# Kernel optimization log

Hardware: AMD Instinct MI355X
Metric: run time of the kernel (lower is better)

Reference implementation:

```python
import jax, jax.numpy as jnp
import numpy as np

T, B, S, A, D = 512, 256, 256, 8, 64
EPS = 1e-6
LOG2PI = float(np.log(2.0 * np.pi))


def setup_inputs() -> dict:
    key = jax.random.key(0)
    ks = jax.random.split(key, 6)
    return {
        "x": jax.random.normal(ks[0], (T, B, D), dtype=jnp.float32),
        "a": jax.random.uniform(ks[1], (T, B, A), dtype=jnp.float32),
        "mask": jnp.ones((T, B), dtype=jnp.float32),
        "mu": jax.random.normal(ks[2], (S, D), dtype=jnp.float32),
        "lv": jax.random.normal(ks[3], (S, D), dtype=jnp.float32) * 0.1,
        "w_logits": jax.random.normal(ks[4], (A, S, S), dtype=jnp.float32),
        "s0_logits": jax.random.normal(ks[5], (S,), dtype=jnp.float32),
    }


def _gauss_log_prob(x, mu, lv):
    # x: [T,B,D], mu/lv: [S,D] -> [T,B,S]; diagonal Gaussian via matmul expansion
    inv_var = jnp.exp(-lv)                                  # [S,D]
    quad = (jnp.einsum('tbd,sd->tbs', x * x, inv_var)
            - 2.0 * jnp.einsum('tbd,sd->tbs', x, mu * inv_var)
            + jnp.sum(mu * mu * inv_var, axis=-1))          # [T,B,S]
    return -0.5 * (quad + jnp.sum(lv, axis=-1) + D * LOG2PI)


def reference(x, a, mask, mu, lv, w_logits, s0_logits):
    trans_all = jax.nn.softmax(w_logits, axis=-1)           # [A,S,S] row-stochastic
    log_pi0 = jax.nn.log_softmax(s0_logits)                 # [S]
    logp_x = _gauss_log_prob(x, mu, lv)                     # [T,B,S]

    # ---- forward (alpha) ----
    b1 = jax.nn.softmax(logp_x[0] + log_pi0[None, :], axis=-1)  # [B,S]

    def fstep(b, inp):
        lx, a_prev = inp
        trans = jnp.einsum('ba,aij->bij', a_prev, trans_all)      # [B,S,S]
        logp_z = jnp.log(jnp.sum(trans * b[:, :, None] + EPS, axis=1))
        b_t = jax.nn.softmax(lx + logp_z, axis=-1)
        return b_t, b_t

    _, alpha_rest = jax.lax.scan(fstep, b1, (logp_x[1:], a[:-1]))
    alpha = jnp.concatenate([b1[None], alpha_rest], axis=0)       # [T,B,S]

    # ---- backward (log beta) ----
    logb_T = jnp.zeros((B, S), dtype=x.dtype)

    def bstep(logb, inp):
        lx, a_prev, m_t = inp
        trans = jnp.einsum('ba,aij->bij', a_prev, trans_all)      # [B,S,S]
        logb_prev = jax.nn.logsumexp(lx[:, None, :] + jnp.log(trans + EPS)
                                     + logb[:, None, :], axis=-1)
        logb_prev = logb_prev * (m_t[:, None] == 1.0)
        return logb_prev, logb_prev

    _, beta_rest = jax.lax.scan(bstep, logb_T, (logp_x[1:], a[:-1], mask[1:]),
                                reverse=True)
    log_beta = jnp.concatenate([beta_rest, logb_T[None]], axis=0)  # [T,B,S]

    # ---- posterior state marginals ----
    q_z = jax.nn.softmax(jnp.log(alpha + EPS) + log_beta, axis=-1)
    return q_z
```

## Files before the change

### kernel.cpp

```cpp
#include <hip/hip_runtime.h>
#include <hip/hip_bf16.h>

#define TT 512
#define BB 256
#define SS 256
#define AA 8
#define DD 64

typedef unsigned short ushort_t;
typedef unsigned long long u64_t;
typedef __bf16 bf16x8 __attribute__((ext_vector_type(8)));
typedef float  f32x4  __attribute__((ext_vector_type(4)));
typedef unsigned int u32x4v __attribute__((ext_vector_type(4)));
typedef unsigned int u32x2v __attribute__((ext_vector_type(2)));

__device__ __forceinline__ ushort_t f2bf(float x) {
  union { float f; unsigned u; } v; v.f = x;
  unsigned r = (v.u + 0x7FFFu + ((v.u >> 16) & 1u)) >> 16;
  return (ushort_t)r;
}
__device__ __forceinline__ float bf2f(unsigned h) {
  return __uint_as_float((h & 0xFFFFu) << 16);
}
__device__ __forceinline__ void st_u32(unsigned* p, unsigned v) {
  __hip_atomic_store(p, v, __ATOMIC_RELAXED, __HIP_MEMORY_SCOPE_AGENT);
}

__device__ __forceinline__ void poll_once(const u64_t* p0, const u64_t* p1,
                                          const u64_t* pcf,
                                          u64_t d[8], unsigned& clo, unsigned& chi) {
  u32x4v a0, a1, a2, a3; u32x2v cf;
  asm volatile(
      "global_load_dwordx4 %0, %5, off sc0 sc1\n\t"
      "global_load_dwordx4 %1, %6, off sc0 sc1\n\t"
      "global_load_dwordx4 %2, %7, off sc0 sc1\n\t"
      "global_load_dwordx4 %3, %8, off sc0 sc1\n\t"
      "global_load_dwordx2 %4, %9, off sc0 sc1\n\t"
      "s_waitcnt vmcnt(0)"
      : "=&v"(a0), "=&v"(a1), "=&v"(a2), "=&v"(a3), "=&v"(cf)
      : "v"(p0), "v"(p0 + 2), "v"(p1), "v"(p1 + 2), "v"(pcf)
      : "memory");
  d[0] = (u64_t)a0[0] | ((u64_t)a0[1] << 32);
  d[1] = (u64_t)a0[2] | ((u64_t)a0[3] << 32);
  d[2] = (u64_t)a1[0] | ((u64_t)a1[1] << 32);
  d[3] = (u64_t)a1[2] | ((u64_t)a1[3] << 32);
  d[4] = (u64_t)a2[0] | ((u64_t)a2[1] << 32);
  d[5] = (u64_t)a2[2] | ((u64_t)a2[3] << 32);
  d[6] = (u64_t)a3[0] | ((u64_t)a3[1] << 32);
  d[7] = (u64_t)a3[2] | ((u64_t)a3[3] << 32);
  clo = cf[0]; chi = cf[1];
}

__global__ __launch_bounds__(64) void k_params(const float* __restrict__ mu,
                                               const float* __restrict__ lv,
                                               float* __restrict__ A1, float* __restrict__ A2,
                                               float* __restrict__ Cs) {
  const float LOG2PI = 1.8378770664093453f;
  int s = blockIdx.x, d = threadIdx.x;
  float l = lv[s * DD + d], m_ = mu[s * DD + d];
  float inv = __expf(-l);
  A1[s * DD + d] = inv;
  A2[s * DD + d] = m_ * inv;
  float part = m_ * m_ * inv + l;
  #pragma unroll
  for (int o = 32; o >= 1; o >>= 1) part += __shfl_down(part, o);
  if (d == 0) Cs[s] = part + (float)DD * LOG2PI;
}

__global__ __launch_bounds__(256) void k_pi0(const float* __restrict__ s0, float* __restrict__ lp0) {
  __shared__ float red[4];
  int tid = threadIdx.x, ln = tid & 63, wv = tid >> 6;
  float v = s0[tid];
  float m = v;
  #pragma unroll
  for (int o = 32; o >= 1; o >>= 1) m = fmaxf(m, __shfl_xor(m, o));
  if (ln == 0) red[wv] = m;
  __syncthreads();
  m = fmaxf(fmaxf(red[0], red[1]), fmaxf(red[2], red[3]));
  __syncthreads();
  float e = __expf(v - m);
  float s = e;
  #pragma unroll
  for (int o = 32; o >= 1; o >>= 1) s += __shfl_xor(s, o);
  if (ln == 0) red[wv] = s;
  __syncthreads();
  s = red[0] + red[1] + red[2] + red[3];
  lp0[tid] = v - m - __logf(s);
}

__global__ __launch_bounds__(256) void k_trans(const float* __restrict__ wl,
                                               ushort_t* __restrict__ Wf, ushort_t* __restrict__ Wb) {
  int tid = threadIdx.x;
  int rl = tid >> 5, l = tid & 31;
  int row = blockIdx.x * 8 + rl;
  int a = row >> 8, i = row & 255;
  const float* src = wl + (size_t)row * 256 + l * 8;
  float v[8];
  *reinterpret_cast<float4*>(&v[0]) = *reinterpret_cast<const float4*>(src);
  *reinterpret_cast<float4*>(&v[4]) = *reinterpret_cast<const float4*>(src + 4);
  float m = v[0];
  #pragma unroll
  for (int k = 1; k < 8; ++k) m = fmaxf(m, v[k]);
  #pragma unroll
  for (int o = 16; o >= 1; o >>= 1) m = fmaxf(m, __shfl_xor(m, o, 32));
  float s = 0.f;
  #pragma unroll
  for (int k = 0; k < 8; ++k) { v[k] = __expf(v[k] - m); s += v[k]; }
  #pragma unroll
  for (int o = 16; o >= 1; o >>= 1) s += __shfl_xor(s, o, 32);
  float inv = 1.0f / s;
  #pragma unroll
  for (int k = 0; k < 8; ++k) {
    int j = l * 8 + k;
    ushort_t h = f2bf(v[k] * inv);
    size_t fi = (size_t)((a * 8 + (i >> 5)) * 16 + (j >> 4));
    Wf[fi * 512 + (((i >> 3) & 3) * 16 + (j & 15)) * 8 + (i & 7)] = h;
    size_t bi = (size_t)((a * 8 + (j >> 5)) * 16 + (i >> 4));
    Wb[bi * 512 + (((j >> 3) & 3) * 16 + (i & 15)) * 8 + (j & 7)] = h;
  }
}

__global__ __launch_bounds__(256) void k_logp(const float* __restrict__ x,
    const float* __restrict__ A1, const float* __restrict__ A2,
    const float* __restrict__ Cs, float* __restrict__ logp, float* __restrict__ Mmax) {
  __shared__ float sA1[64][64];
  __shared__ float sA2[64][64];
  int tid = threadIdx.x;
  int row = tid >> 3, dg = tid & 7;
  size_t row0 = (size_t)blockIdx.x * 32;
  const float* xp = x + (row0 + row) * DD + dg * 8;
  float xv[8];
  *reinterpret_cast<float4*>(&xv[0]) = *reinterpret_cast<const float4*>(xp);
  *reinterpret_cast<float4*>(&xv[4]) = *reinterpret_cast<const float4*>(xp + 4);
  float m = -3.0e38f;
  float* orow = logp + (row0 + row) * SS;
  for (int st = 0; st < 4; ++st) {
    __syncthreads();
    #pragma unroll
    for (int k = 0; k < 4; ++k) {
      int flat = k * 1024 + tid * 4;
      int sr = flat >> 6, sc = flat & 63;
      *reinterpret_cast<float4*>(&sA1[sr][sc]) = *reinterpret_cast<const float4*>(&A1[(size_t)(st * 64 + sr) * 64 + sc]);
      *reinterpret_cast<float4*>(&sA2[sr][sc]) = *reinterpret_cast<const float4*>(&A2[(size_t)(st * 64 + sr) * 64 + sc]);
    }
    __syncthreads();
    for (int s = 0; s < 64; ++s) {
      float acc = 0.f;
      #pragma unroll
      for (int j = 0; j < 8; ++j) {
        float t1 = __builtin_fmaf(sA1[s][dg * 8 + j], xv[j], -2.0f * sA2[s][dg * 8 + j]);
        acc = __builtin_fmaf(t1, xv[j], acc);
      }
      acc += __shfl_xor(acc, 1, 8);
      acc += __shfl_xor(acc, 2, 8);
      acc += __shfl_xor(acc, 4, 8);
      float lp = -0.5f * (acc + Cs[st * 64 + s]);
      m = fmaxf(m, lp);
      if (((s ^ dg) & 7) == 0) orow[st * 64 + s] = lp;
    }
  }
  if (dg == 0) Mmax[row0 + row] = m;
}

__global__ __launch_bounds__(256, 1) void k_recur(
    const float* __restrict__ a_in, const float* __restrict__ mask,
    float* __restrict__ out, float* __restrict__ beta,
    const float* __restrict__ logp, const float* __restrict__ Mmax,
    float* __restrict__ cpart,
    const ushort_t* __restrict__ Wf, const ushort_t* __restrict__ Wb,
    const float* __restrict__ lp0,
    unsigned* __restrict__ amb, unsigned* __restrict__ bmb,
    unsigned* __restrict__ cmb, unsigned* __restrict__ rmb) {
  const float EPSF  = 1e-6f;
  const float EPS_S = 256.0f * 1e-6f;
  const int tid  = threadIdx.x;
  const int lane = tid & 63;
  const int wave = tid >> 6;
  const int xcd  = blockIdx.x & 7;
  const int slot = blockIdx.x >> 3;
  const int wg   = slot & 7;
  const int grpg = (slot >> 3) * 8 + xcd;
  const bool isF = (grpg < 16);
  const int grp  = grpg & 15;
  const int b0   = grp * 16;
  const int jc0  = wg * 32;

  __shared__ float yred[2][4][2][64][4];
  __shared__ float rowUp[2][4][16];

  bf16x8 bfrag[8][2][2];
  {
    const ushort_t* Ws = isF ? Wf : Wb;
    #pragma unroll
    for (int a = 0; a < 8; ++a)
      #pragma unroll
      for (int kk = 0; kk < 2; ++kk)
        #pragma unroll
        for (int nt = 0; nt < 2; ++nt) {
          const int kc = wave * 2 + kk;
          const int fragid = (a * 8 + kc) * 16 + wg * 2 + nt;
          bfrag[a][kk][nt] = *reinterpret_cast<const bf16x8*>(Ws + (size_t)fragid * 512 + lane * 8);
        }
  }

  const int m_ = lane & 15;
  const int q_ = lane >> 4;
  const int frow = tid >> 4;
  const int fcol = tid & 15;
  const int lsrc = (frow >> 2) * 16 + fcol;
  const int rg_  = frow & 3;
  const u64_t TAGMASK = 0xFFFF0000FFFF0000ULL;
  const size_t fpub = (size_t)(frow & 7) * 16 + wg * 2 + (frow >> 3);

  if (isF) {
    {
      float mm = Mmax[b0 + frow];
      float csum = 0.f;
      #pragma unroll
      for (int nt = 0; nt < 2; ++nt) {
        int j = jc0 + nt * 16 + fcol;
        float lx = logp[(size_t)(b0 + frow) * SS + j];
        float v = __expf(lx - mm + lp0[j]);
        st_u32(&amb[((size_t)(0 * 16 + grp) * 16 + frow) * 256 + j], (unsigned)f2bf(v));
        out[(size_t)(b0 + frow) * SS + j] = v;
        csum += v;
      }
      #pragma unroll
      for (int o = 8; o >= 1; o >>= 1) csum += __shfl_down(csum, o, 16);
      if (fcol == 0) {
        st_u32(&cmb[((size_t)(0 * 16 + grp)) * 128 + fpub], (unsigned)f2bf(csum));
        cpart[((size_t)grp * 16 + frow) * 8 + wg] = csum;
      }
    }

    for (int t = 1; t < TT; ++t) {
      const int par_r = (t - 1) & 1, par_w = t & 1;
      float wcur[4][8];
      {
        const float* ab = a_in + ((size_t)(t - 1) * BB + b0 + q_ * 4) * AA;
        #pragma unroll
        for (int r = 0; r < 4; ++r) {
          *reinterpret_cast<float4*>(&wcur[r][0]) = *reinterpret_cast<const float4*>(ab + r * AA);
          *reinterpret_cast<float4*>(&wcur[r][4]) = *reinterpret_cast<const float4*>(ab + r * AA + 4);
        }
      }
      float mmn = Mmax[(size_t)t * BB + b0 + frow];
      const float* lsp = logp + ((size_t)t * BB + b0 + frow) * SS + jc0;
      float ex0 = __expf(lsp[fcol] - mmn);
      float ex1 = __expf(lsp[16 + fcol] - mmn);

      const u64_t* pr = (const u64_t*)(amb + (((size_t)par_r * 16 + grp) * 16 + m_) * 256);
      const u64_t* p0 = pr + wave * 32 + q_ * 4;
      const u64_t* p1 = p0 + 16;
      const u64_t* pcf = (const u64_t*)cmb + ((size_t)par_r * 16 + grp) * 64 + (lane >> 3) * 8 + (lane & 7);
      const unsigned tg = (unsigned)(t - 1);
      const u64_t pat = ((u64_t)tg << 48) | ((u64_t)tg << 16);
      u64_t d[8]; unsigned clo, chi;
      while (true) {
        poll_once(p0, p1, pcf, d, clo, chi);
        bool ok = ((clo >> 16) == tg) & ((chi >> 16) == tg);
        #pragma unroll
        for (int k = 0; k < 8; ++k) ok &= ((d[k] & TAGMASK) == pat);
        if (__all(ok)) break;
      }
      float slo = bf2f(clo), shi = bf2f(chi);
      slo += __shfl_xor(slo, 4, 8); slo += __shfl_xor(slo, 2, 8); slo += __shfl_xor(slo, 1, 8);
      shi += __shfl_xor(shi, 4, 8); shi += __shfl_xor(shi, 2, 8); shi += __shfl_xor(shi, 1, 8);
      float vlo = __shfl(slo, (m_ & 7) * 8);
      float vhi = __shfl(shi, (m_ & 7) * 8);
      float ra = 1.0f / ((m_ < 8) ? vlo : vhi);

      float ys[2][4] = {{0.f,0.f,0.f,0.f},{0.f,0.f,0.f,0.f}};
      {
        bf16x8 af0, af1;
        #pragma unroll
        for (int e = 0; e < 8; ++e) {
          unsigned h0 = (e & 1) ? (unsigned)(d[e >> 1] >> 32) : (unsigned)d[e >> 1];
          unsigned h1 = (e & 1) ? (unsigned)(d[4 + (e >> 1)] >> 32) : (unsigned)d[4 + (e >> 1)];
          af0[e] = (__bf16)(bf2f(h0) * ra);
          af1[e] = (__bf16)(bf2f(h1) * ra);
        }
        #pragma unroll
        for (int a = 0; a < 8; ++a) {
          #pragma unroll
          for (int nt = 0; nt < 2; ++nt) {
            f32x4 c = {0.f, 0.f, 0.f, 0.f};
            c = __builtin_amdgcn_mfma_f32_16x16x32_bf16(af0, bfrag[a][0][nt], c, 0, 0, 0);
            c = __builtin_amdgcn_mfma_f32_16x16x32_bf16(af1, bfrag[a][1][nt], c, 0, 0, 0);
            #pragma unroll
            for (int r = 0; r < 4; ++r) ys[nt][r] += wcur[r][a] * c[r];
          }
        }
      }
      #pragma unroll
      for (int nt = 0; nt < 2; ++nt)
        *reinterpret_cast<float4*>(&yred[par_w][wave][nt][lane][0]) =
            make_float4(ys[nt][0], ys[nt][1], ys[nt][2], ys[nt][3]);
      __syncthreads();
      {
        float* orow = out + ((size_t)t * BB + b0 + frow) * SS + jc0;
        unsigned* mrow = amb + (((size_t)par_w * 16 + grp) * 16 + frow) * 256 + jc0;
        float y0 = yred[par_w][0][0][lsrc][rg_] + yred[par_w][1][0][lsrc][rg_] +
                   yred[par_w][2][0][lsrc][rg_] + yred[par_w][3][0][lsrc][rg_];
        float y1 = yred[par_w][0][1][lsrc][rg_] + yred[par_w][1][1][lsrc][rg_] +
                   yred[par_w][2][1][lsrc][rg_] + yred[par_w][3][1][lsrc][rg_];
        float bh0 = ex0 * (y0 + EPS_S);
        float bh1 = ex1 * (y1 + EPS_S);
        st_u32(mrow + fcol, ((unsigned)t << 16) | f2bf(bh0));
        st_u32(mrow + 16 + fcol, ((unsigned)t << 16) | f2bf(bh1));
        float csum = bh0 + bh1;
        #pragma unroll
        for (int o = 8; o >= 1; o >>= 1) csum += __shfl_down(csum, o, 16);
        if (fcol == 0)
          st_u32(&cmb[((size_t)par_w * 16 + grp) * 128 + fpub],
                 ((unsigned)t << 16) | f2bf(csum));
        orow[fcol] = bh0;
        orow[16 + fcol] = bh1;
        if (fcol == 0) {
          float cs = __shfl(csum, (tid >> 4) * 16, 64);
          cpart[(((size_t)t * 16 + grp) * 16 + frow) * 8 + wg] = cs;
        }
      }
    }
  } else {
    {
      const unsigned tg0 = (unsigned)(TT - 1);
      float* brow = beta + ((size_t)(TT - 1) * BB + b0 + frow) * SS + jc0;
      unsigned* mrow = bmb + (((size_t)((TT - 1) & 1) * 16 + grp) * 16 + frow) * 256 + jc0;
      st_u32(mrow + fcol, (tg0 << 16) | 0x3F80u);
      st_u32(mrow + 16 + fcol, (tg0 << 16) | 0x3F80u);
      brow[fcol] = 1.0f; brow[16 + fcol] = 1.0f;
      if (fcol == 0)
        st_u32(&rmb[((size_t)((TT - 1) & 1) * 16 + grp) * 128 + fpub],
               (tg0 << 16) | f2bf(32.0f));
    }

    for (int t = TT - 2; t >= 0; --t) {
      const int tr = t + 1;
      const int par_r = tr & 1, par_w = t & 1;
      float wcur[4][8];
      {
        const float* ab = a_in + ((size_t)t * BB + b0 + q_ * 4) * AA;
        #pragma unroll
        for (int r = 0; r < 4; ++r) {
          *reinterpret_cast<float4*>(&wcur[r][0]) = *reinterpret_cast<const float4*>(ab + r * AA);
          *reinterpret_cast<float4*>(&wcur[r][4]) = *reinterpret_cast<const float4*>(ab + r * AA + 4);
        }
      }
      float lp0v[8], lp1v[8];
      {
        const float* lrow = logp + ((size_t)tr * BB + b0 + m_) * SS + wave * 64 + q_ * 8;
        *reinterpret_cast<float4*>(&lp0v[0]) = *reinterpret_cast<const float4*>(lrow);
        *reinterpret_cast<float4*>(&lp0v[4]) = *reinterpret_cast<const float4*>(lrow + 4);
        *reinterpret_cast<float4*>(&lp1v[0]) = *reinterpret_cast<const float4*>(lrow + 32);
        *reinterpret_cast<float4*>(&lp1v[4]) = *reinterpret_cast<const float4*>(lrow + 36);
      }
      float mm_ = Mmax[(size_t)tr * BB + b0 + m_];
      float mk  = mask[(size_t)tr * BB + b0 + frow];

      const u64_t* pr = (const u64_t*)(bmb + (((size_t)par_r * 16 + grp) * 16 + m_) * 256);
      const u64_t* p0 = pr + wave * 32 + q_ * 4;
      const u64_t* p1 = p0 + 16;
      const u64_t* pcf = (const u64_t*)rmb + ((size_t)par_r * 16 + grp) * 64 + (lane >> 3) * 8 + (lane & 7);
      const unsigned tg = (unsigned)tr;
      const u64_t pat = ((u64_t)tg << 48) | ((u64_t)tg << 16);
      u64_t d[8]; unsigned clo, chi;
      while (true) {
        poll_once(p0, p1, pcf, d, clo, chi);
        bool ok = ((clo >> 16) == tg) & ((chi >> 16) == tg);
        #pragma unroll
        for (int k = 0; k < 8; ++k) ok &= ((d[k] & TAGMASK) == pat);
        if (__all(ok)) break;
      }
      float slo = bf2f(clo), shi = bf2f(chi);
      slo += __shfl_xor(slo, 4, 8); slo += __shfl_xor(slo, 2, 8); slo += __shfl_xor(slo, 1, 8);
      shi += __shfl_xor(shi, 4, 8); shi += __shfl_xor(shi, 2, 8); shi += __shfl_xor(shi, 1, 8);
      float vlo = __shfl(slo, (m_ & 7) * 8);
      float vhi = __shfl(shi, (m_ & 7) * 8);
      float ri = 1.0f / ((m_ < 8) ? vlo : vhi);
      float vloF = __shfl(slo, (frow & 7) * 8);
      float vhiF = __shfl(shi, (frow & 7) * 8);
      float riF = 1.0f / ((frow < 8) ? vloF : vhiF);

      float partial = 0.f;
      float ys[2][4] = {{0.f,0.f,0.f,0.f},{0.f,0.f,0.f,0.f}};
      {
        bf16x8 af0, af1;
        #pragma unroll
        for (int e = 0; e < 8; ++e) {
          unsigned h0 = (e & 1) ? (unsigned)(d[e >> 1] >> 32) : (unsigned)d[e >> 1];
          unsigned h1 = (e & 1) ? (unsigned)(d[4 + (e >> 1)] >> 32) : (unsigned)d[4 + (e >> 1)];
          float g0 = __expf(lp0v[e] - mm_) * bf2f(h0);
          float g1 = __expf(lp1v[e] - mm_) * bf2f(h1);
          partial += g0 + g1;
          af0[e] = (__bf16)(g0 * ri);
          af1[e] = (__bf16)(g1 * ri);
        }
        #pragma unroll
        for (int a = 0; a < 8; ++a) {
          #pragma unroll
          for (int nt = 0; nt < 2; ++nt) {
            f32x4 c = {0.f, 0.f, 0.f, 0.f};
            c = __builtin_amdgcn_mfma_f32_16x16x32_bf16(af0, bfrag[a][0][nt], c, 0, 0, 0);
            c = __builtin_amdgcn_mfma_f32_16x16x32_bf16(af1, bfrag[a][1][nt], c, 0, 0, 0);
            #pragma unroll
            for (int r = 0; r < 4; ++r) ys[nt][r] += wcur[r][a] * c[r];
          }
        }
      }
      partial += __shfl_xor(partial, 16);
      partial += __shfl_xor(partial, 32);
      if (q_ == 0) rowUp[par_w][wave][m_] = partial;
      #pragma unroll
      for (int nt = 0; nt < 2; ++nt)
        *reinterpret_cast<float4*>(&yred[par_w][wave][nt][lane][0]) =
            make_float4(ys[nt][0], ys[nt][1], ys[nt][2], ys[nt][3]);
      __syncthreads();
      {
        float rowU = rowUp[par_w][0][frow] + rowUp[par_w][1][frow] +
                     rowUp[par_w][2][frow] + rowUp[par_w][3][frow];
        float eg = EPSF * riF * rowU;
        bool mk1 = (mk == 1.0f);
        float* brow = beta + ((size_t)t * BB + b0 + frow) * SS + jc0;
        unsigned* mrow = bmb + (((size_t)par_w * 16 + grp) * 16 + frow) * 256 + jc0;
        float y0 = yred[par_w][0][0][lsrc][rg_] + yred[par_w][1][0][lsrc][rg_] +
                   yred[par_w][2][0][lsrc][rg_] + yred[par_w][3][0][lsrc][rg_];
        float y1 = yred[par_w][0][1][lsrc][rg_] + yred[par_w][1][1][lsrc][rg_] +
                   yred[par_w][2][1][lsrc][rg_] + yred[par_w][3][1][lsrc][rg_];
        float v0 = mk1 ? (y0 + eg) : 1.0f;
        float v1 = mk1 ? (y1 + eg) : 1.0f;
        st_u32(mrow + fcol, ((unsigned)t << 16) | f2bf(v0));
        st_u32(mrow + 16 + fcol, ((unsigned)t << 16) | f2bf(v1));
        float rsum = v0 + v1;
        #pragma unroll
        for (int o = 8; o >= 1; o >>= 1) rsum += __shfl_down(rsum, o, 16);
        if (fcol == 0)
          st_u32(&rmb[((size_t)par_w * 16 + grp) * 128 + fpub],
                 ((unsigned)t << 16) | f2bf(rsum));
        brow[fcol] = v0;
        brow[16 + fcol] = v1;
      }
    }
  }
}

__global__ __launch_bounds__(256) void k_qz(float* __restrict__ out,
    const float* __restrict__ beta, const float* __restrict__ cpart) {
  const float EPSF = 1e-6f;
  int tid = threadIdx.x;
  size_t row = (size_t)blockIdx.x * 8 + (tid >> 5);
  int l = tid & 31;
  int tt = (int)(row >> 8);
  int b  = (int)(row & 255);
  int grp = b >> 4, r = b & 15;
  float pv = 0.f;
  if (l < 8) pv = cpart[(((size_t)tt * 16 + grp) * 16 + r) * 8 + l];
  pv += __shfl_down(pv, 4, 8); pv += __shfl_down(pv, 2, 8); pv += __shfl_down(pv, 1, 8);
  float ce = __shfl(pv, 0, 32) * EPSF;
  float* po = out + row * SS + l * 8;
  const float* pb = beta + row * SS + l * 8;
  float4 v0 = *reinterpret_cast<const float4*>(po);
  float4 v1 = *reinterpret_cast<const float4*>(po + 4);
  float4 b0 = *reinterpret_cast<const float4*>(pb);
  float4 b1 = *reinterpret_cast<const float4*>(pb + 4);
  float z[8];
  z[0] = __logf(v0.x + ce) + __logf(b0.x);
  z[1] = __logf(v0.y + ce) + __logf(b0.y);
  z[2] = __logf(v0.z + ce) + __logf(b0.z);
  z[3] = __logf(v0.w + ce) + __logf(b0.w);
  z[4] = __logf(v1.x + ce) + __logf(b1.x);
  z[5] = __logf(v1.y + ce) + __logf(b1.y);
  z[6] = __logf(v1.z + ce) + __logf(b1.z);
  z[7] = __logf(v1.w + ce) + __logf(b1.w);
  float m = z[0];
  #pragma unroll
  for (int k = 1; k < 8; ++k) m = fmaxf(m, z[k]);
  #pragma unroll
  for (int o = 16; o >= 1; o >>= 1) m = fmaxf(m, __shfl_xor(m, o, 32));
  float e[8]; float s = 0.f;
  #pragma unroll
  for (int k = 0; k < 8; ++k) { e[k] = __expf(z[k] - m); s += e[k]; }
  #pragma unroll
  for (int o = 16; o >= 1; o >>= 1) s += __shfl_xor(s, o, 32);
  float inv = 1.0f / s;
  *reinterpret_cast<float4*>(po)     = make_float4(e[0]*inv, e[1]*inv, e[2]*inv, e[3]*inv);
  *reinterpret_cast<float4*>(po + 4) = make_float4(e[4]*inv, e[5]*inv, e[6]*inv, e[7]*inv);
}

extern "C" void kernel_launch(void* const* d_in, const int* in_sizes, int n_in,
                              void* d_out, int out_size, void* d_ws, size_t ws_size,
                              hipStream_t stream) {
  (void)in_sizes; (void)n_in; (void)out_size;
  const float* x   = (const float*)d_in[0];
  const float* a   = (const float*)d_in[1];
  const float* msk = (const float*)d_in[2];
  const float* mu  = (const float*)d_in[3];
  const float* lv  = (const float*)d_in[4];
  const float* wl  = (const float*)d_in[5];
  const float* s0  = (const float*)d_in[6];
  float* out = (float*)d_out;

  char* ws = (char*)d_ws;
  float* logp  = (float*)ws;  ws += (size_t)TT * BB * SS * 4;
  float* beta  = (float*)ws;  ws += (size_t)TT * BB * SS * 4;
  float* Mmax  = (float*)ws;  ws += (size_t)TT * BB * 4;
  float* cpart = (float*)ws;  ws += (size_t)TT * BB * 8 * 4;
  ushort_t* Wf = (ushort_t*)ws; ws += (size_t)AA * SS * SS * 2;
  ushort_t* Wb = (ushort_t*)ws; ws += (size_t)AA * SS * SS * 2;
  float* A1 = (float*)ws;    ws += (size_t)SS * DD * 4;
  float* A2 = (float*)ws;    ws += (size_t)SS * DD * 4;
  float* Cs = (float*)ws;    ws += 1024;
  float* lp0 = (float*)ws;   ws += 1024;
  unsigned* amb = (unsigned*)ws; ws += (size_t)2 * 16 * 16 * 256 * 4;
  unsigned* bmb = (unsigned*)ws; ws += (size_t)2 * 16 * 16 * 256 * 4;
  unsigned* cmb = (unsigned*)ws; ws += (size_t)2 * 16 * 16 * 8 * 4;
  unsigned* rmb = (unsigned*)ws; ws += (size_t)2 * 16 * 16 * 8 * 4;
  if (ws_size < (size_t)(ws - (char*)d_ws)) return;

  hipMemsetAsync(amb, 0xFF, (size_t)(2 * 16 * 16 * 256 * 4) * 2 + (size_t)(2 * 16 * 16 * 8 * 4) * 2, stream);

  k_params<<<SS, DD, 0, stream>>>(mu, lv, A1, A2, Cs);
  k_pi0<<<1, SS, 0, stream>>>(s0, lp0);
  k_trans<<<256, 256, 0, stream>>>(wl, Wf, Wb);
  k_logp<<<TT * BB / 32, 256, 0, stream>>>(x, A1, A2, Cs, logp, Mmax);
  k_recur<<<256, 256, 0, stream>>>(a, msk, out, beta, logp, Mmax, cpart, Wf, Wb, lp0,
                                   amb, bmb, cmb, rmb);
  k_qz<<<TT * BB / 8, 256, 0, stream>>>(out, beta, cpart);
}
```

Baseline: 2.076 ms.

## Defer row-sum normalization past the MFMA to take flag polling off the critical path

The recurrence loop used to poll the message data and the per-row normalization sums together, then scale the A operand before running the MFMAs. Now it polls only the data, runs the MFMAs on unscaled values, and polls the row-sum flags after the block barrier. The reciprocal is applied to the reduced output instead, in both the forward and backward chains. This aims to overlap the wait for the sums with the matrix work and to drop per-element scaling before the MFMA, at the cost of a second polling loop and a change in bf16 rounding order. The backward exp terms are also hoisted ahead of the poll, and the cmb/rmb workspace sizes were corrected (the new sizes are the same).

```diff
diff --git a/kernel.cpp b/kernel.cpp
--- a/kernel.cpp
+++ b/kernel.cpp
@@ -13,6 +13,7 @@
 typedef float  f32x4  __attribute__((ext_vector_type(4)));
 typedef unsigned int u32x4v __attribute__((ext_vector_type(4)));
 typedef unsigned int u32x2v __attribute__((ext_vector_type(2)));
+typedef short short8v __attribute__((ext_vector_type(8)));
 
 __device__ __forceinline__ ushort_t f2bf(float x) {
   union { float f; unsigned u; } v; v.f = x;
@@ -26,19 +27,16 @@
   __hip_atomic_store(p, v, __ATOMIC_RELAXED, __HIP_MEMORY_SCOPE_AGENT);
 }
 
-__device__ __forceinline__ void poll_once(const u64_t* p0, const u64_t* p1,
-                                          const u64_t* pcf,
-                                          u64_t d[8], unsigned& clo, unsigned& chi) {
-  u32x4v a0, a1, a2, a3; u32x2v cf;
+__device__ __forceinline__ void poll_data(const u64_t* p0, const u64_t* p1, u64_t d[8]) {
+  u32x4v a0, a1, a2, a3;
   asm volatile(
-      "global_load_dwordx4 %0, %5, off sc0 sc1\n\t"
-      "global_load_dwordx4 %1, %6, off sc0 sc1\n\t"
-      "global_load_dwordx4 %2, %7, off sc0 sc1\n\t"
-      "global_load_dwordx4 %3, %8, off sc0 sc1\n\t"
-      "global_load_dwordx2 %4, %9, off sc0 sc1\n\t"
+      "global_load_dwordx4 %0, %4, off sc0 sc1\n\t"
+      "global_load_dwordx4 %1, %5, off sc0 sc1\n\t"
+      "global_load_dwordx4 %2, %6, off sc0 sc1\n\t"
+      "global_load_dwordx4 %3, %7, off sc0 sc1\n\t"
       "s_waitcnt vmcnt(0)"
-      : "=&v"(a0), "=&v"(a1), "=&v"(a2), "=&v"(a3), "=&v"(cf)
-      : "v"(p0), "v"(p0 + 2), "v"(p1), "v"(p1 + 2), "v"(pcf)
+      : "=&v"(a0), "=&v"(a1), "=&v"(a2), "=&v"(a3)
+      : "v"(p0), "v"(p0 + 2), "v"(p1), "v"(p1 + 2)
       : "memory");
   d[0] = (u64_t)a0[0] | ((u64_t)a0[1] << 32);
   d[1] = (u64_t)a0[2] | ((u64_t)a0[3] << 32);
@@ -48,6 +46,13 @@
   d[5] = (u64_t)a2[2] | ((u64_t)a2[3] << 32);
   d[6] = (u64_t)a3[0] | ((u64_t)a3[1] << 32);
   d[7] = (u64_t)a3[2] | ((u64_t)a3[3] << 32);
+}
+__device__ __forceinline__ void poll_flags(const u64_t* pcf, unsigned& clo, unsigned& chi) {
+  u32x2v cf;
+  asm volatile(
+      "global_load_dwordx2 %0, %1, off sc0 sc1\n\t"
+      "s_waitcnt vmcnt(0)"
+      : "=&v"(cf) : "v"(pcf) : "memory");
   clo = cf[0]; chi = cf[1];
 }
 
@@ -255,41 +260,38 @@
       const u64_t* pcf = (const u64_t*)cmb + ((size_t)par_r * 16 + grp) * 64 + (lane >> 3) * 8 + (lane & 7);
       const unsigned tg = (unsigned)(t - 1);
       const u64_t pat = ((u64_t)tg << 48) | ((u64_t)tg << 16);
-      u64_t d[8]; unsigned clo, chi;
+      u64_t d[8];
       while (true) {
-        poll_once(p0, p1, pcf, d, clo, chi);
-        bool ok = ((clo >> 16) == tg) & ((chi >> 16) == tg);
+        poll_data(p0, p1, d);
+        bool ok = true;
         #pragma unroll
         for (int k = 0; k < 8; ++k) ok &= ((d[k] & TAGMASK) == pat);
         if (__all(ok)) break;
       }
-      float slo = bf2f(clo), shi = bf2f(chi);
-      slo += __shfl_xor(slo, 4, 8); slo += __shfl_xor(slo, 2, 8); slo += __shfl_xor(slo, 1, 8);
-      shi += __shfl_xor(shi, 4, 8); shi += __shfl_xor(shi, 2, 8); shi += __shfl_xor(shi, 1, 8);
-      float vlo = __shfl(slo, (m_ & 7) * 8);
-      float vhi = __shfl(shi, (m_ & 7) * 8);
-      float ra = 1.0f / ((m_ < 8) ? vlo : vhi);
-
-      float ys[2][4] = {{0.f,0.f,0.f,0.f},{0.f,0.f,0.f,0.f}};
+      bf16x8 af0, af1;
       {
-        bf16x8 af0, af1;
+        short8v s0v, s1v;
         #pragma unroll
         for (int e = 0; e < 8; ++e) {
           unsigned h0 = (e & 1) ? (unsigned)(d[e >> 1] >> 32) : (unsigned)d[e >> 1];
           unsigned h1 = (e & 1) ? (unsigned)(d[4 + (e >> 1)] >> 32) : (unsigned)d[4 + (e >> 1)];
-          af0[e] = (__bf16)(bf2f(h0) * ra);
-          af1[e] = (__bf16)(bf2f(h1) * ra);
-        }
-        #pragma unroll
-        for (int a = 0; a < 8; ++a) {
+          s0v[e] = (short)(h0 & 0xFFFFu);
+          s1v[e] = (short)(h1 & 0xFFFFu);
+        }
+        af0 = *reinterpret_cast<bf16x8*>(&s0v);
+        af1 = *reinterpret_cast<bf16x8*>(&s1v);
+      }
+
+      float ys[2][4] = {{0.f,0.f,0.f,0.f},{0.f,0.f,0.f,0.f}};
+      #pragma unroll
+      for (int a = 0; a < 8; ++a) {
+        #pragma unroll
+        for (int nt = 0; nt < 2; ++nt) {
+          f32x4 c = {0.f, 0.f, 0.f, 0.f};
+          c = __builtin_amdgcn_mfma_f32_16x16x32_bf16(af0, bfrag[a][0][nt], c, 0, 0, 0);
+          c = __builtin_amdgcn_mfma_f32_16x16x32_bf16(af1, bfrag[a][1][nt], c, 0, 0, 0);
           #pragma unroll
-          for (int nt = 0; nt < 2; ++nt) {
-            f32x4 c = {0.f, 0.f, 0.f, 0.f};
-            c = __builtin_amdgcn_mfma_f32_16x16x32_bf16(af0, bfrag[a][0][nt], c, 0, 0, 0);
-            c = __builtin_amdgcn_mfma_f32_16x16x32_bf16(af1, bfrag[a][1][nt], c, 0, 0, 0);
-            #pragma unroll
-            for (int r = 0; r < 4; ++r) ys[nt][r] += wcur[r][a] * c[r];
-          }
+          for (int r = 0; r < 4; ++r) ys[nt][r] += wcur[r][a] * c[r];
         }
       }
       #pragma unroll
@@ -298,14 +300,26 @@
             make_float4(ys[nt][0], ys[nt][1], ys[nt][2], ys[nt][3]);
       __syncthreads();
       {
+        unsigned clo, chi;
+        while (true) {
+          poll_flags(pcf, clo, chi);
+          if (__all(((clo >> 16) == tg) & ((chi >> 16) == tg))) break;
+        }
+        float slo = bf2f(clo), shi = bf2f(chi);
+        slo += __shfl_xor(slo, 4, 8); slo += __shfl_xor(slo, 2, 8); slo += __shfl_xor(slo, 1, 8);
+        shi += __shfl_xor(shi, 4, 8); shi += __shfl_xor(shi, 2, 8); shi += __shfl_xor(shi, 1, 8);
+        float clo_ = __shfl(slo, (frow & 7) * 8);
+        float chi_ = __shfl(shi, (frow & 7) * 8);
+        float raF = 1.0f / ((frow < 8) ? clo_ : chi_);
+
         float* orow = out + ((size_t)t * BB + b0 + frow) * SS + jc0;
         unsigned* mrow = amb + (((size_t)par_w * 16 + grp) * 16 + frow) * 256 + jc0;
         float y0 = yred[par_w][0][0][lsrc][rg_] + yred[par_w][1][0][lsrc][rg_] +
                    yred[par_w][2][0][lsrc][rg_] + yred[par_w][3][0][lsrc][rg_];
         float y1 = yred[par_w][0][1][lsrc][rg_] + yred[par_w][1][1][lsrc][rg_] +
                    yred[par_w][2][1][lsrc][rg_] + yred[par_w][3][1][lsrc][rg_];
-        float bh0 = ex0 * (y0 + EPS_S);
-        float bh1 = ex1 * (y1 + EPS_S);
+        float bh0 = ex0 * (__builtin_fmaf(raF, y0, EPS_S));
+        float bh1 = ex1 * (__builtin_fmaf(raF, y1, EPS_S));
         st_u32(mrow + fcol, ((unsigned)t << 16) | f2bf(bh0));
         st_u32(mrow + 16 + fcol, ((unsigned)t << 16) | f2bf(bh1));
         float csum = bh0 + bh1;
@@ -316,10 +330,8 @@
                  ((unsigned)t << 16) | f2bf(csum));
         orow[fcol] = bh0;
         orow[16 + fcol] = bh1;
-        if (fcol == 0) {
-          float cs = __shfl(csum, (tid >> 4) * 16, 64);
-          cpart[(((size_t)t * 16 + grp) * 16 + frow) * 8 + wg] = cs;
-        }
+        if (fcol == 0)
+          cpart[(((size_t)t * 16 + grp) * 16 + frow) * 8 + wg] = csum;
       }
     }
   } else {
@@ -357,6 +369,12 @@
       }
       float mm_ = Mmax[(size_t)tr * BB + b0 + m_];
       float mk  = mask[(size_t)tr * BB + b0 + frow];
+      float eg0[8], eg1[8];
+      #pragma unroll
+      for (int e = 0; e < 8; ++e) {
+        eg0[e] = __expf(lp0v[e] - mm_);
+        eg1[e] = __expf(lp1v[e] - mm_);
+      }
 
       const u64_t* pr = (const u64_t*)(bmb + (((size_t)par_r * 16 + grp) * 16 + m_) * 256);
       const u64_t* p0 = pr + wave * 32 + q_ * 4;
@@ -364,48 +382,37 @@
       const u64_t* pcf = (const u64_t*)rmb + ((size_t)par_r * 16 + grp) * 64 + (lane >> 3) * 8 + (lane & 7);
       const unsigned tg = (unsigned)tr;
       const u64_t pat = ((u64_t)tg << 48) | ((u64_t)tg << 16);
-      u64_t d[8]; unsigned clo, chi;
+      u64_t d[8];
       while (true) {
-        poll_once(p0, p1, pcf, d, clo, chi);
-        bool ok = ((clo >> 16) == tg) & ((chi >> 16) == tg);
+        poll_data(p0, p1, d);
+        bool ok = true;
         #pragma unroll
         for (int k = 0; k < 8; ++k) ok &= ((d[k] & TAGMASK) == pat);
         if (__all(ok)) break;
       }
-      float slo = bf2f(clo), shi = bf2f(chi);
-      slo += __shfl_xor(slo, 4, 8); slo += __shfl_xor(slo, 2, 8); slo += __shfl_xor(slo, 1, 8);
-      shi += __shfl_xor(shi, 4, 8); shi += __shfl_xor(shi, 2, 8); shi += __shfl_xor(shi, 1, 8);
-      float vlo = __shfl(slo, (m_ & 7) * 8);
-      float vhi = __shfl(shi, (m_ & 7) * 8);
-      float ri = 1.0f / ((m_ < 8) ? vlo : vhi);
-      float vloF = __shfl(slo, (frow & 7) * 8);
-      float vhiF = __shfl(shi, (frow & 7) * 8);
-      float riF = 1.0f / ((frow < 8) ? vloF : vhiF);
 
       float partial = 0.f;
+      bf16x8 af0, af1;
+      #pragma unroll
+      for (int e = 0; e < 8; ++e) {
+        unsigned h0 = (e & 1) ? (unsigned)(d[e >> 1] >> 32) : (unsigned)d[e >> 1];
+        unsigned h1 = (e & 1) ? (unsigned)(d[4 + (e >> 1)] >> 32) : (unsigned)d[4 + (e >> 1)];
+        float g0 = eg0[e] * bf2f(h0);
+        float g1 = eg1[e] * bf2f(h1);
+        partial += g0 + g1;
+        af0[e] = (__bf16)g0;
+        af1[e] = (__bf16)g1;
+      }
       float ys[2][4] = {{0.f,0.f,0.f,0.f},{0.f,0.f,0.f,0.f}};
-      {
-        bf16x8 af0, af1;
-        #pragma unroll
-        for (int e = 0; e < 8; ++e) {
-          unsigned h0 = (e & 1) ? (unsigned)(d[e >> 1] >> 32) : (unsigned)d[e >> 1];
-          unsigned h1 = (e & 1) ? (unsigned)(d[4 + (e >> 1)] >> 32) : (unsigned)d[4 + (e >> 1)];
-          float g0 = __expf(lp0v[e] - mm_) * bf2f(h0);
-          float g1 = __expf(lp1v[e] - mm_) * bf2f(h1);
-          partial += g0 + g1;
-          af0[e] = (__bf16)(g0 * ri);
-          af1[e] = (__bf16)(g1 * ri);
-        }
-        #pragma unroll
-        for (int a = 0; a < 8; ++a) {
+      #pragma unroll
+      for (int a = 0; a < 8; ++a) {
+        #pragma unroll
+        for (int nt = 0; nt < 2; ++nt) {
+          f32x4 c = {0.f, 0.f, 0.f, 0.f};
+          c = __builtin_amdgcn_mfma_f32_16x16x32_bf16(af0, bfrag[a][0][nt], c, 0, 0, 0);
+          c = __builtin_amdgcn_mfma_f32_16x16x32_bf16(af1, bfrag[a][1][nt], c, 0, 0, 0);
           #pragma unroll
-          for (int nt = 0; nt < 2; ++nt) {
-            f32x4 c = {0.f, 0.f, 0.f, 0.f};
-            c = __builtin_amdgcn_mfma_f32_16x16x32_bf16(af0, bfrag[a][0][nt], c, 0, 0, 0);
-            c = __builtin_amdgcn_mfma_f32_16x16x32_bf16(af1, bfrag[a][1][nt], c, 0, 0, 0);
-            #pragma unroll
-            for (int r = 0; r < 4; ++r) ys[nt][r] += wcur[r][a] * c[r];
-          }
+          for (int r = 0; r < 4; ++r) ys[nt][r] += wcur[r][a] * c[r];
         }
       }
       partial += __shfl_xor(partial, 16);
@@ -417,9 +424,20 @@
             make_float4(ys[nt][0], ys[nt][1], ys[nt][2], ys[nt][3]);
       __syncthreads();
       {
+        unsigned clo, chi;
+        while (true) {
+          poll_flags(pcf, clo, chi);
+          if (__all(((clo >> 16) == tg) & ((chi >> 16) == tg))) break;
+        }
+        float slo = bf2f(clo), shi = bf2f(chi);
+        slo += __shfl_xor(slo, 4, 8); slo += __shfl_xor(slo, 2, 8); slo += __shfl_xor(slo, 1, 8);
+        shi += __shfl_xor(shi, 4, 8); shi += __shfl_xor(shi, 2, 8); shi += __shfl_xor(shi, 1, 8);
+        float vloF = __shfl(slo, (frow & 7) * 8);
+        float vhiF = __shfl(shi, (frow & 7) * 8);
+        float riF = 1.0f / ((frow < 8) ? vloF : vhiF);
+
         float rowU = rowUp[par_w][0][frow] + rowUp[par_w][1][frow] +
                      rowUp[par_w][2][frow] + rowUp[par_w][3][frow];
-        float eg = EPSF * riF * rowU;
         bool mk1 = (mk == 1.0f);
         float* brow = beta + ((size_t)t * BB + b0 + frow) * SS + jc0;
         unsigned* mrow = bmb + (((size_t)par_w * 16 + grp) * 16 + frow) * 256 + jc0;
@@ -427,8 +445,8 @@
                    yred[par_w][2][0][lsrc][rg_] + yred[par_w][3][0][lsrc][rg_];
         float y1 = yred[par_w][0][1][lsrc][rg_] + yred[par_w][1][1][lsrc][rg_] +
                    yred[par_w][2][1][lsrc][rg_] + yred[par_w][3][1][lsrc][rg_];
-        float v0 = mk1 ? (y0 + eg) : 1.0f;
-        float v1 = mk1 ? (y1 + eg) : 1.0f;
+        float v0 = mk1 ? riF * (__builtin_fmaf(EPSF, rowU, y0)) : 1.0f;
+        float v1 = mk1 ? riF * (__builtin_fmaf(EPSF, rowU, y1)) : 1.0f;
         st_u32(mrow + fcol, ((unsigned)t << 16) | f2bf(v0));
         st_u32(mrow + 16 + fcol, ((unsigned)t << 16) | f2bf(v1));
         float rsum = v0 + v1;
@@ -513,11 +531,12 @@
   float* lp0 = (float*)ws;   ws += 1024;
   unsigned* amb = (unsigned*)ws; ws += (size_t)2 * 16 * 16 * 256 * 4;
   unsigned* bmb = (unsigned*)ws; ws += (size_t)2 * 16 * 16 * 256 * 4;
-  unsigned* cmb = (unsigned*)ws; ws += (size_t)2 * 16 * 16 * 8 * 4;
-  unsigned* rmb = (unsigned*)ws; ws += (size_t)2 * 16 * 16 * 8 * 4;
+  unsigned* cmb = (unsigned*)ws; ws += (size_t)2 * 16 * 128 * 4;
+  unsigned* rmb = (unsigned*)ws; ws += (size_t)2 * 16 * 128 * 4;
   if (ws_size < (size_t)(ws - (char*)d_ws)) return;
 
-  hipMemsetAsync(amb, 0xFF, (size_t)(2 * 16 * 16 * 256 * 4) * 2 + (size_t)(2 * 16 * 16 * 8 * 4) * 2, stream);
+  hipMemsetAsync(amb, 0xFF, (size_t)(2 * 16 * 16 * 256 * 4) * 2
+                           + (size_t)(2 * 16 * 128 * 4) * 2, stream);
 
   k_params<<<SS, DD, 0, stream>>>(mu, lv, A1, A2, Cs);
   k_pi0<<<1, SS, 0, stream>>>(s0, lp0);
```

After: 2.122 ms. +2.2%, slower.
